# Optimization experiments

Measured on AMD Instinct MI355X. Metric: run time of the kernel, lower is better.

## Reference

```python
import jax, jax.numpy as jnp
import numpy as np

IN, OUT, S = 4096, 4096, 256
B, T = 4, 2048

# Straight-through-estimator sign quantizer (binary quant of low-rank factors).
@jax.custom_vjp
def ste_sign(x):
    return jnp.sign(x)

def _ste_fwd(x):
    return jnp.sign(x), None

def _ste_bwd(_, g):
    return (g,)

ste_sign.defvjp(_ste_fwd, _ste_bwd)


def setup_inputs() -> dict:
    key = jax.random.key(0)
    ks = jax.random.split(key, 14)
    nrm = lambda k, shp, s: jax.random.normal(k, shp, dtype=jnp.float32) * s
    uni = lambda k, shp: jax.random.uniform(k, shp, dtype=jnp.float32, minval=0.1, maxval=1.0)
    return {
        "x": nrm(ks[0], (B, T, IN), 1.0),
        "V": nrm(ks[1], (S, IN), 0.02),
        "U": nrm(ks[2], (OUT, S), 0.02),
        "v1": uni(ks[3], (1, S)),
        "v2": uni(ks[4], (1, IN)),
        "u1": uni(ks[5], (1, OUT)),
        "u2": uni(ks[6], (1, S)),
        "V_R": nrm(ks[7], (S, IN), 0.02),
        "U_R": nrm(ks[8], (OUT, S), 0.02),
        "v1_R": uni(ks[9], (1, S)),
        "v2_R": uni(ks[10], (1, IN)),
        "u1_R": uni(ks[11], (1, OUT)),
        "u2_R": uni(ks[12], (1, S)),
        "bias": nrm(ks[13], (OUT,), 0.02),
    }


def _branch(x2, V, U, v1, v2, u1, u2):
    # y = (((x * v2) @ sign(V).T) * (v1*u2)) @ sign(U).T * u1   (left-to-right, as in torch)
    Vq = ste_sign(V)          # [S, IN]
    Uq = ste_sign(U)          # [OUT, S]
    h = (x2 * v2) @ Vq.T      # [N, S]
    h = h * (v1 * u2)         # per-rank scale
    y = h @ Uq.T              # [N, OUT]
    return y * u1


def reference(x, V, U, v1, v2, u1, u2, V_R, U_R, v1_R, v2_R, u1_R, u2_R, bias):
    shp = x.shape
    x2 = x.reshape(-1, shp[-1])                                  # [N, IN]
    y = _branch(x2, V, U, v1, v2, u1, u2)
    y = y + _branch(x2, V_R, U_R, v1_R, v2_R, u1_R, u2_R)        # residual low-rank branch
    y = y + bias
    return y.reshape(shp[:-1] + (OUT,))
```

## Files before the change

kernel.cpp:

```cpp
#include <hip/hip_runtime.h>
#include <hip/hip_bf16.h>
#include <stdint.h>
#include <stddef.h>

typedef __attribute__((ext_vector_type(8))) short short8;
typedef __attribute__((ext_vector_type(4))) float floatx4;

#define AS_GLOBAL(p) (const __attribute__((address_space(1))) void*)(p)
#define AS_LDS(p)    (__attribute__((address_space(3))) void*)(p)

static constexpr int IN_DIM  = 4096;
static constexpr int OUT_DIM = 4096;
static constexpr int S_DIM   = 256;
static constexpr int S2      = 512;


__global__ void build_w1_kernel(const float* __restrict__ V, const float* __restrict__ v2,
                                const float* __restrict__ V_R, const float* __restrict__ v2_R,
                                __hip_bfloat16* __restrict__ W1) {
  const int idx = blockIdx.x * 256 + threadIdx.x;
  const int i = idx & (IN_DIM - 1);
  const int s = idx >> 12;
  float w, sc;
  if (s < S_DIM) { w = V[s * IN_DIM + i];            sc = v2[i]; }
  else           { w = V_R[(s - S_DIM) * IN_DIM + i]; sc = v2_R[i]; }
  const float sg = (w > 0.f) ? 1.f : ((w < 0.f) ? -1.f : 0.f);
  W1[idx] = __float2bfloat16(sg * sc);
}

__global__ void build_w2_kernel(const float* __restrict__ U, const float* __restrict__ u1,
                                const float* __restrict__ v1, const float* __restrict__ u2,
                                const float* __restrict__ U_R, const float* __restrict__ u1_R,
                                const float* __restrict__ v1_R, const float* __restrict__ u2_R,
                                __hip_bfloat16* __restrict__ W2) {
  const int idx = blockIdx.x * 256 + threadIdx.x;
  const int s = idx & (S2 - 1);
  const int o = idx >> 9;
  float w, sc;
  if (s < S_DIM) { w = U[o * S_DIM + s];   sc = u1[o] * v1[s] * u2[s]; }
  else { const int ss = s - S_DIM; w = U_R[o * S_DIM + ss]; sc = u1_R[o] * v1_R[ss] * u2_R[ss]; }
  const float sg = (w > 0.f) ? 1.f : ((w < 0.f) ? -1.f : 0.f);
  W2[idx] = __float2bfloat16(sg * sc);
}

__global__ __launch_bounds__(256, 2)
void gemm1_kernel(const float* __restrict__ A,
                  const __hip_bfloat16* __restrict__ B,
                  __hip_bfloat16* __restrict__ C) {
  constexpr int K = IN_DIM;
  constexpr int N = S2;
  constexpr int BM = 64, BN = 128, BK = 32;

  __shared__ float As[BM * BK];
  __shared__ __hip_bfloat16 Bs[BN * BK];

  const int t = threadIdx.x;
  const int wave = t >> 6;
  const int lane = t & 63;
  const int r16 = lane & 15;
  const int quad = lane >> 4;

  const int f = blockIdx.x;
  const int xcd = f & 7;
  const int l = f >> 3;
  const int tm0 = (xcd * 16 + (l & 15)) * BM;
  const int tn0 = (l >> 4) * BN;

  const int wm = (wave & 1) * 32;
  const int wn = (wave >> 1) * 64;

  floatx4 acc[2][4] = {};

  for (int k0 = 0; k0 < K; k0 += BK) {
#pragma unroll
    for (int i = 0; i < 2; ++i) {
      const int p = t + i * 256;
      const int row = p >> 3;
      const int ql = (p & 7) ^ (row & 7);
      const float* gp = A + (size_t)(tm0 + row) * K + k0 + ql * 4;
      __builtin_amdgcn_global_load_lds(AS_GLOBAL(gp), AS_LDS((char*)As + p * 16), 16, 0, 0);
    }
#pragma unroll
    for (int i = 0; i < 2; ++i) {
      const int p = t + i * 256;
      const int row = p >> 2;
      const int q = p & 3;
      const __hip_bfloat16* gp = B + (size_t)(tn0 + row) * K + k0 + q * 8;
      __builtin_amdgcn_global_load_lds(AS_GLOBAL(gp), AS_LDS((char*)Bs + p * 16), 16, 0, 0);
    }
    __syncthreads();

    short8 a[2];
    short8 b[4];
#pragma unroll
    for (int i = 0; i < 2; ++i) {
      const int ar = wm + i * 16 + r16;
      const int p0 = ar * 8 + ((quad * 2) ^ (ar & 7));
      const int p1 = ar * 8 + ((quad * 2 + 1) ^ (ar & 7));
      const floatx4 f0 = *reinterpret_cast<const floatx4*>((const char*)As + p0 * 16);
      const floatx4 f1 = *reinterpret_cast<const floatx4*>((const char*)As + p1 * 16);
      union { short8 v; __hip_bfloat16 h[8]; } u;
      u.h[0] = __float2bfloat16(f0.x); u.h[1] = __float2bfloat16(f0.y);
      u.h[2] = __float2bfloat16(f0.z); u.h[3] = __float2bfloat16(f0.w);
      u.h[4] = __float2bfloat16(f1.x); u.h[5] = __float2bfloat16(f1.y);
      u.h[6] = __float2bfloat16(f1.z); u.h[7] = __float2bfloat16(f1.w);
      a[i] = u.v;
    }
#pragma unroll
    for (int j = 0; j < 4; ++j) {
      const int br = wn + j * 16 + r16;
      b[j] = *reinterpret_cast<const short8*>((const char*)Bs + br * 64 + quad * 16);
    }
#pragma unroll
    for (int i = 0; i < 2; ++i)
#pragma unroll
      for (int j = 0; j < 4; ++j)
        acc[i][j] = __builtin_amdgcn_mfma_f32_16x16x32_bf16(a[i], b[j], acc[i][j], 0, 0, 0);
    __syncthreads();
  }

#pragma unroll
  for (int i = 0; i < 2; ++i)
#pragma unroll
    for (int j = 0; j < 4; ++j)
#pragma unroll
      for (int r = 0; r < 4; ++r) {
        const int row = tm0 + wm + i * 16 + quad * 4 + r;
        const int col = tn0 + wn + j * 16 + r16;
        C[(size_t)row * N + col] = __float2bfloat16(acc[i][j][r]);
      }
}

__global__ __launch_bounds__(256, 2)
void gemm2_kernel(const __hip_bfloat16* __restrict__ A,
                  const __hip_bfloat16* __restrict__ B,
                  const float* __restrict__ bias,
                  float* __restrict__ C) {
  constexpr int K = S2;
  constexpr int N = OUT_DIM;
  constexpr int BM = 128, BN = 128, BK = 32;

  __shared__ __hip_bfloat16 As[BM * BK];
  __shared__ __hip_bfloat16 Bs[BN * BK];

  const int t = threadIdx.x;
  const int wave = t >> 6;
  const int lane = t & 63;
  const int r16 = lane & 15;
  const int quad = lane >> 4;

  const int tm0 = blockIdx.y * BM;
  const int tn0 = blockIdx.x * BN;

  const int wm = (wave & 1) * 64;
  const int wn = (wave >> 1) * 64;

  floatx4 acc[4][4] = {};

  for (int k0 = 0; k0 < K; k0 += BK) {
#pragma unroll
    for (int i = 0; i < 2; ++i) {
      const int p = t + i * 256;
      const int row = p >> 2;
      const int q = p & 3;
      const __hip_bfloat16* gp = A + (size_t)(tm0 + row) * K + k0 + q * 8;
      __builtin_amdgcn_global_load_lds(AS_GLOBAL(gp), AS_LDS((char*)As + p * 16), 16, 0, 0);
    }
#pragma unroll
    for (int i = 0; i < 2; ++i) {
      const int p = t + i * 256;
      const int row = p >> 2;
      const int q = p & 3;
      const __hip_bfloat16* gp = B + (size_t)(tn0 + row) * K + k0 + q * 8;
      __builtin_amdgcn_global_load_lds(AS_GLOBAL(gp), AS_LDS((char*)Bs + p * 16), 16, 0, 0);
    }
    __syncthreads();

    short8 a[4], b[4];
#pragma unroll
    for (int i = 0; i < 4; ++i) {
      const int ar = wm + i * 16 + r16;
      a[i] = *reinterpret_cast<const short8*>((const char*)As + ar * 64 + quad * 16);
    }
#pragma unroll
    for (int j = 0; j < 4; ++j) {
      const int br = wn + j * 16 + r16;
      b[j] = *reinterpret_cast<const short8*>((const char*)Bs + br * 64 + quad * 16);
    }
#pragma unroll
    for (int i = 0; i < 4; ++i)
#pragma unroll
      for (int j = 0; j < 4; ++j)
        acc[i][j] = __builtin_amdgcn_mfma_f32_16x16x32_bf16(a[i], b[j], acc[i][j], 0, 0, 0);
    __syncthreads();
  }

#pragma unroll
  for (int i = 0; i < 4; ++i)
#pragma unroll
    for (int j = 0; j < 4; ++j)
#pragma unroll
      for (int r = 0; r < 4; ++r) {
        const int row = tm0 + wm + i * 16 + quad * 4 + r;
        const int col = tn0 + wn + j * 16 + r16;
        C[(size_t)row * N + col] = acc[i][j][r] + bias[col];
      }
}

extern "C" void kernel_launch(void* const* d_in, const int* in_sizes, int n_in,
                              void* d_out, int out_size, void* d_ws, size_t ws_size,
                              hipStream_t stream) {
  const float* x    = (const float*)d_in[0];
  const float* V    = (const float*)d_in[1];
  const float* U    = (const float*)d_in[2];
  const float* v1   = (const float*)d_in[3];
  const float* v2   = (const float*)d_in[4];
  const float* u1   = (const float*)d_in[5];
  const float* u2   = (const float*)d_in[6];
  const float* V_R  = (const float*)d_in[7];
  const float* U_R  = (const float*)d_in[8];
  const float* v1_R = (const float*)d_in[9];
  const float* v2_R = (const float*)d_in[10];
  const float* u1_R = (const float*)d_in[11];
  const float* u2_R = (const float*)d_in[12];
  const float* bias = (const float*)d_in[13];
  float* out = (float*)d_out;

  const int M = in_sizes[0] / IN_DIM;

  char* ws = (char*)d_ws;
  __hip_bfloat16* W1 = (__hip_bfloat16*)ws;
  __hip_bfloat16* W2 = (__hip_bfloat16*)(ws + (size_t)S2 * IN_DIM * 2);
  __hip_bfloat16* H  = (__hip_bfloat16*)(ws + (size_t)S2 * IN_DIM * 4);

  build_w1_kernel<<<(S2 * IN_DIM) / 256, 256, 0, stream>>>(V, v2, V_R, v2_R, W1);
  build_w2_kernel<<<(OUT_DIM * S2) / 256, 256, 0, stream>>>(U, u1, v1, u2, U_R, u1_R, v1_R, u2_R, W2);

  gemm1_kernel<<<(M / 64) * (S2 / 128), 256, 0, stream>>>(x, W1, H);

  gemm2_kernel<<<dim3(OUT_DIM / 128, M / 128), 256, 0, stream>>>(H, W2, bias, out);
}
```

Measured before the change: 390.7 us.

## Pre-convert x to bf16, retile both GEMMs with BK=64, vectorize weight builds

```diff
diff --git a/kernel.cpp b/kernel.cpp
--- a/kernel.cpp
+++ b/kernel.cpp
@@ -18,14 +18,24 @@
 __global__ void build_w1_kernel(const float* __restrict__ V, const float* __restrict__ v2,
                                 const float* __restrict__ V_R, const float* __restrict__ v2_R,
                                 __hip_bfloat16* __restrict__ W1) {
-  const int idx = blockIdx.x * 256 + threadIdx.x;
-  const int i = idx & (IN_DIM - 1);
-  const int s = idx >> 12;
-  float w, sc;
-  if (s < S_DIM) { w = V[s * IN_DIM + i];            sc = v2[i]; }
-  else           { w = V_R[(s - S_DIM) * IN_DIM + i]; sc = v2_R[i]; }
-  const float sg = (w > 0.f) ? 1.f : ((w < 0.f) ? -1.f : 0.f);
-  W1[idx] = __float2bfloat16(sg * sc);
+  const int idx4 = (blockIdx.x * 256 + threadIdx.x) * 4;
+  const int i = idx4 & (IN_DIM - 1);
+  const int s = idx4 >> 12;
+  floatx4 w, sc;
+  if (s < S_DIM) {
+    w  = *(const floatx4*)(V + s * IN_DIM + i);
+    sc = *(const floatx4*)(v2 + i);
+  } else {
+    w  = *(const floatx4*)(V_R + (s - S_DIM) * IN_DIM + i);
+    sc = *(const floatx4*)(v2_R + i);
+  }
+  union { ushort4 v; __hip_bfloat16 h[4]; } u;
+#pragma unroll
+  for (int j = 0; j < 4; ++j) {
+    const float sg = (w[j] > 0.f) ? 1.f : ((w[j] < 0.f) ? -1.f : 0.f);
+    u.h[j] = __float2bfloat16(sg * sc[j]);
+  }
+  *(ushort4*)((unsigned short*)W1 + idx4) = u.v;
 }
 
 __global__ void build_w2_kernel(const float* __restrict__ U, const float* __restrict__ u1,
@@ -33,25 +43,55 @@
                                 const float* __restrict__ U_R, const float* __restrict__ u1_R,
                                 const float* __restrict__ v1_R, const float* __restrict__ u2_R,
                                 __hip_bfloat16* __restrict__ W2) {
+  const int idx4 = (blockIdx.x * 256 + threadIdx.x) * 4;
+  const int s = idx4 & (S2 - 1);
+  const int o = idx4 >> 9;
+  floatx4 w, scs;
+  float sco;
+  if (s < S_DIM) {
+    w   = *(const floatx4*)(U + o * S_DIM + s);
+    sco = u1[o];
+    const floatx4 a = *(const floatx4*)(v1 + s);
+    const floatx4 b = *(const floatx4*)(u2 + s);
+    scs = a * b;
+  } else {
+    const int ss = s - S_DIM;
+    w   = *(const floatx4*)(U_R + o * S_DIM + ss);
+    sco = u1_R[o];
+    const floatx4 a = *(const floatx4*)(v1_R + ss);
+    const floatx4 b = *(const floatx4*)(u2_R + ss);
+    scs = a * b;
+  }
+  union { ushort4 v; __hip_bfloat16 h[4]; } u;
+#pragma unroll
+  for (int j = 0; j < 4; ++j) {
+    const float sg = (w[j] > 0.f) ? 1.f : ((w[j] < 0.f) ? -1.f : 0.f);
+    u.h[j] = __float2bfloat16(sg * sco * scs[j]);
+  }
+  *(ushort4*)((unsigned short*)W2 + idx4) = u.v;
+}
+
+__global__ void cvt_x_kernel(const float* __restrict__ x, __hip_bfloat16* __restrict__ xb) {
   const int idx = blockIdx.x * 256 + threadIdx.x;
-  const int s = idx & (S2 - 1);
-  const int o = idx >> 9;
-  float w, sc;
-  if (s < S_DIM) { w = U[o * S_DIM + s];   sc = u1[o] * v1[s] * u2[s]; }
-  else { const int ss = s - S_DIM; w = U_R[o * S_DIM + ss]; sc = u1_R[o] * v1_R[ss] * u2_R[ss]; }
-  const float sg = (w > 0.f) ? 1.f : ((w < 0.f) ? -1.f : 0.f);
-  W2[idx] = __float2bfloat16(sg * sc);
+  const floatx4 f0 = *((const floatx4*)x + idx * 2);
+  const floatx4 f1 = *((const floatx4*)x + idx * 2 + 1);
+  union { short8 v; __hip_bfloat16 h[8]; } u;
+  u.h[0] = __float2bfloat16(f0.x); u.h[1] = __float2bfloat16(f0.y);
+  u.h[2] = __float2bfloat16(f0.z); u.h[3] = __float2bfloat16(f0.w);
+  u.h[4] = __float2bfloat16(f1.x); u.h[5] = __float2bfloat16(f1.y);
+  u.h[6] = __float2bfloat16(f1.z); u.h[7] = __float2bfloat16(f1.w);
+  *((short8*)xb + idx) = u.v;
 }
 
 __global__ __launch_bounds__(256, 2)
-void gemm1_kernel(const float* __restrict__ A,
+void gemm1_kernel(const __hip_bfloat16* __restrict__ A,
                   const __hip_bfloat16* __restrict__ B,
                   __hip_bfloat16* __restrict__ C) {
   constexpr int K = IN_DIM;
   constexpr int N = S2;
-  constexpr int BM = 64, BN = 128, BK = 32;
-
-  __shared__ float As[BM * BK];
+  constexpr int BM = 128, BN = 64, BK = 64;
+
+  __shared__ __hip_bfloat16 As[BM * BK];
   __shared__ __hip_bfloat16 Bs[BN * BK];
 
   const int t = threadIdx.x;
@@ -61,68 +101,62 @@
   const int quad = lane >> 4;
 
   const int f = blockIdx.x;
-  const int xcd = f & 7;
+  const int c = f & 7;
   const int l = f >> 3;
-  const int tm0 = (xcd * 16 + (l & 15)) * BM;
-  const int tn0 = (l >> 4) * BN;
-
-  const int wm = (wave & 1) * 32;
-  const int wn = (wave >> 1) * 64;
-
-  floatx4 acc[2][4] = {};
+  const int tm0 = (c * 8 + (l >> 3)) * BM;
+  const int tn0 = (l & 7) * BN;
+
+  const int wm = (wave & 1) * 64;
+  const int wn = (wave >> 1) * 32;
+
+  floatx4 acc[4][2] = {};
 
   for (int k0 = 0; k0 < K; k0 += BK) {
 #pragma unroll
+    for (int i = 0; i < 4; ++i) {
+      const int p = t + i * 256;
+      const int row = p >> 3;
+      const int ql = (p & 7) ^ (row & 7);
+      const __hip_bfloat16* gp = A + (size_t)(tm0 + row) * K + k0 + ql * 8;
+      __builtin_amdgcn_global_load_lds(AS_GLOBAL(gp), AS_LDS((char*)As + p * 16), 16, 0, 0);
+    }
+#pragma unroll
     for (int i = 0; i < 2; ++i) {
       const int p = t + i * 256;
       const int row = p >> 3;
       const int ql = (p & 7) ^ (row & 7);
-      const float* gp = A + (size_t)(tm0 + row) * K + k0 + ql * 4;
-      __builtin_amdgcn_global_load_lds(AS_GLOBAL(gp), AS_LDS((char*)As + p * 16), 16, 0, 0);
-    }
-#pragma unroll
-    for (int i = 0; i < 2; ++i) {
-      const int p = t + i * 256;
-      const int row = p >> 2;
-      const int q = p & 3;
-      const __hip_bfloat16* gp = B + (size_t)(tn0 + row) * K + k0 + q * 8;
+      const __hip_bfloat16* gp = B + (size_t)(tn0 + row) * K + k0 + ql * 8;
       __builtin_amdgcn_global_load_lds(AS_GLOBAL(gp), AS_LDS((char*)Bs + p * 16), 16, 0, 0);
     }
     __syncthreads();
 
-    short8 a[2];
-    short8 b[4];
-#pragma unroll
-    for (int i = 0; i < 2; ++i) {
-      const int ar = wm + i * 16 + r16;
-      const int p0 = ar * 8 + ((quad * 2) ^ (ar & 7));
-      const int p1 = ar * 8 + ((quad * 2 + 1) ^ (ar & 7));
-      const floatx4 f0 = *reinterpret_cast<const floatx4*>((const char*)As + p0 * 16);
-      const floatx4 f1 = *reinterpret_cast<const floatx4*>((const char*)As + p1 * 16);
-      union { short8 v; __hip_bfloat16 h[8]; } u;
-      u.h[0] = __float2bfloat16(f0.x); u.h[1] = __float2bfloat16(f0.y);
-      u.h[2] = __float2bfloat16(f0.z); u.h[3] = __float2bfloat16(f0.w);
-      u.h[4] = __float2bfloat16(f1.x); u.h[5] = __float2bfloat16(f1.y);
-      u.h[6] = __float2bfloat16(f1.z); u.h[7] = __float2bfloat16(f1.w);
-      a[i] = u.v;
-    }
-#pragma unroll
-    for (int j = 0; j < 4; ++j) {
-      const int br = wn + j * 16 + r16;
-      b[j] = *reinterpret_cast<const short8*>((const char*)Bs + br * 64 + quad * 16);
-    }
-#pragma unroll
-    for (int i = 0; i < 2; ++i)
-#pragma unroll
-      for (int j = 0; j < 4; ++j)
-        acc[i][j] = __builtin_amdgcn_mfma_f32_16x16x32_bf16(a[i], b[j], acc[i][j], 0, 0, 0);
-    __syncthreads();
-  }
-
-#pragma unroll
-  for (int i = 0; i < 2; ++i)
-#pragma unroll
-    for (int j = 0; j < 4; ++j)
+#pragma unroll
+    for (int ks = 0; ks < 2; ++ks) {
+      short8 a[4], b[2];
+      const int cc = ks * 4 + quad;
+#pragma unroll
+      for (int i = 0; i < 4; ++i) {
+        const int ar = wm + i * 16 + r16;
+        a[i] = *reinterpret_cast<const short8*>((const char*)As + (ar * 8 + (cc ^ (ar & 7))) * 16);
+      }
+#pragma unroll
+      for (int j = 0; j < 2; ++j) {
+        const int br = wn + j * 16 + r16;
+        b[j] = *reinterpret_cast<const short8*>((const char*)Bs + (br * 8 + (cc ^ (br & 7))) * 16);
+      }
+#pragma unroll
+      for (int i = 0; i < 4; ++i)
+#pragma unroll
+        for (int j = 0; j < 2; ++j)
+          acc[i][j] = __builtin_amdgcn_mfma_f32_16x16x32_bf16(a[i], b[j], acc[i][j], 0, 0, 0);
+    }
+    __syncthreads();
+  }
+
+#pragma unroll
+  for (int i = 0; i < 4; ++i)
+#pragma unroll
+    for (int j = 0; j < 2; ++j)
 #pragma unroll
       for (int r = 0; r < 4; ++r) {
         const int row = tm0 + wm + i * 16 + quad * 4 + r;
@@ -138,7 +172,7 @@
                   float* __restrict__ C) {
   constexpr int K = S2;
   constexpr int N = OUT_DIM;
-  constexpr int BM = 128, BN = 128, BK = 32;
+  constexpr int BM = 128, BN = 128, BK = 64;
 
   __shared__ __hip_bfloat16 As[BM * BK];
   __shared__ __hip_bfloat16 Bs[BN * BK];
@@ -149,8 +183,11 @@
   const int r16 = lane & 15;
   const int quad = lane >> 4;
 
-  const int tm0 = blockIdx.y * BM;
-  const int tn0 = blockIdx.x * BN;
+  const int f = blockIdx.x;
+  const int c = f & 7;
+  const int l = f >> 3;
+  const int tm0 = (c * 8 + (l >> 5)) * BM;
+  const int tn0 = (l & 31) * BN;
 
   const int wm = (wave & 1) * 64;
   const int wn = (wave >> 1) * 64;
@@ -159,41 +196,49 @@
 
   for (int k0 = 0; k0 < K; k0 += BK) {
 #pragma unroll
-    for (int i = 0; i < 2; ++i) {
-      const int p = t + i * 256;
-      const int row = p >> 2;
-      const int q = p & 3;
-      const __hip_bfloat16* gp = A + (size_t)(tm0 + row) * K + k0 + q * 8;
+    for (int i = 0; i < 4; ++i) {
+      const int p = t + i * 256;
+      const int row = p >> 3;
+      const int ql = (p & 7) ^ (row & 7);
+      const __hip_bfloat16* gp = A + (size_t)(tm0 + row) * K + k0 + ql * 8;
       __builtin_amdgcn_global_load_lds(AS_GLOBAL(gp), AS_LDS((char*)As + p * 16), 16, 0, 0);
     }
 #pragma unroll
-    for (int i = 0; i < 2; ++i) {
-      const int p = t + i * 256;
-      const int row = p >> 2;
-      const int q = p & 3;
-      const __hip_bfloat16* gp = B + (size_t)(tn0 + row) * K + k0 + q * 8;
+    for (int i = 0; i < 4; ++i) {
+      const int p = t + i * 256;
+      const int row = p >> 3;
+      const int ql = (p & 7) ^ (row & 7);
+      const __hip_bfloat16* gp = B + (size_t)(tn0 + row) * K + k0 + ql * 8;
       __builtin_amdgcn_global_load_lds(AS_GLOBAL(gp), AS_LDS((char*)Bs + p * 16), 16, 0, 0);
     }
     __syncthreads();
 
-    short8 a[4], b[4];
-#pragma unroll
-    for (int i = 0; i < 4; ++i) {
-      const int ar = wm + i * 16 + r16;
-      a[i] = *reinterpret_cast<const short8*>((const char*)As + ar * 64 + quad * 16);
-    }
-#pragma unroll
-    for (int j = 0; j < 4; ++j) {
-      const int br = wn + j * 16 + r16;
-      b[j] = *reinterpret_cast<const short8*>((const char*)Bs + br * 64 + quad * 16);
-    }
-#pragma unroll
-    for (int i = 0; i < 4; ++i)
-#pragma unroll
-      for (int j = 0; j < 4; ++j)
-        acc[i][j] = __builtin_amdgcn_mfma_f32_16x16x32_bf16(a[i], b[j], acc[i][j], 0, 0, 0);
-    __syncthreads();
-  }
+#pragma unroll
+    for (int ks = 0; ks < 2; ++ks) {
+      short8 a[4], b[4];
+      const int cc = ks * 4 + quad;
+#pragma unroll
+      for (int i = 0; i < 4; ++i) {
+        const int ar = wm + i * 16 + r16;
+        a[i] = *reinterpret_cast<const short8*>((const char*)As + (ar * 8 + (cc ^ (ar & 7))) * 16);
+      }
+#pragma unroll
+      for (int j = 0; j < 4; ++j) {
+        const int br = wn + j * 16 + r16;
+        b[j] = *reinterpret_cast<const short8*>((const char*)Bs + (br * 8 + (cc ^ (br & 7))) * 16);
+      }
+#pragma unroll
+      for (int i = 0; i < 4; ++i)
+#pragma unroll
+        for (int j = 0; j < 4; ++j)
+          acc[i][j] = __builtin_amdgcn_mfma_f32_16x16x32_bf16(a[i], b[j], acc[i][j], 0, 0, 0);
+    }
+    __syncthreads();
+  }
+
+  float bi[4];
+#pragma unroll
+  for (int j = 0; j < 4; ++j) bi[j] = bias[tn0 + wn + j * 16 + r16];
 
 #pragma unroll
   for (int i = 0; i < 4; ++i)
@@ -203,7 +248,7 @@
       for (int r = 0; r < 4; ++r) {
         const int row = tm0 + wm + i * 16 + quad * 4 + r;
         const int col = tn0 + wn + j * 16 + r16;
-        C[(size_t)row * N + col] = acc[i][j][r] + bias[col];
+        C[(size_t)row * N + col] = acc[i][j][r] + bi[j];
       }
 }
 
@@ -230,13 +275,15 @@
 
   char* ws = (char*)d_ws;
   __hip_bfloat16* W1 = (__hip_bfloat16*)ws;
-  __hip_bfloat16* W2 = (__hip_bfloat16*)(ws + (size_t)S2 * IN_DIM * 2);
-  __hip_bfloat16* H  = (__hip_bfloat16*)(ws + (size_t)S2 * IN_DIM * 4);
-
-  build_w1_kernel<<<(S2 * IN_DIM) / 256, 256, 0, stream>>>(V, v2, V_R, v2_R, W1);
-  build_w2_kernel<<<(OUT_DIM * S2) / 256, 256, 0, stream>>>(U, u1, v1, u2, U_R, u1_R, v1_R, u2_R, W2);
-
-  gemm1_kernel<<<(M / 64) * (S2 / 128), 256, 0, stream>>>(x, W1, H);
-
-  gemm2_kernel<<<dim3(OUT_DIM / 128, M / 128), 256, 0, stream>>>(H, W2, bias, out);
-}
+  __hip_bfloat16* W2 = (__hip_bfloat16*)(ws + (size_t)4 * 1024 * 1024);
+  __hip_bfloat16* H  = (__hip_bfloat16*)(ws + (size_t)8 * 1024 * 1024);
+  __hip_bfloat16* Xb = (__hip_bfloat16*)(ws + (size_t)16 * 1024 * 1024);
+
+  build_w1_kernel<<<(S2 * IN_DIM) / 1024, 256, 0, stream>>>(V, v2, V_R, v2_R, W1);
+  build_w2_kernel<<<(OUT_DIM * S2) / 1024, 256, 0, stream>>>(U, u1, v1, u2, U_R, u1_R, v1_R, u2_R, W2);
+  cvt_x_kernel<<<(M * IN_DIM) / (8 * 256), 256, 0, stream>>>(x, Xb);
+
+  gemm1_kernel<<<(M / 128) * (S2 / 64), 256, 0, stream>>>(Xb, W1, H);
+
+  gemm2_kernel<<<(M / 128) * (OUT_DIM / 128), 256, 0, stream>>>(H, W2, bias, out);
+}
```

Result: faster. 351.1 us (-10.1%).
